# Kernel optimization log

Hardware: AMD Instinct MI355X
Metric: run time of the kernel (lower is better)

## Reference

```python
import jax, jax.numpy as jnp
import numpy as np

N, F, H, R, B, L, C, E, NB = 8192, 512, 256, 16, 32, 256, 7, 262144, 30
D = F + H


def setup_inputs() -> dict:
    ks = jax.random.split(jax.random.key(0), 16)
    g = lambda k, shape, fan: jax.random.normal(k, shape, jnp.float32) / np.sqrt(fan)
    return {
        "x": jax.random.normal(ks[0], (N, F), jnp.float32),
        "edge_index": jax.random.randint(ks[1], (2, E), 0, N),
        "edge_norm": jax.random.uniform(ks[2], (E,), jnp.float32),
        "edge_type": jax.random.randint(ks[3], (E,), 0, R),
        "seq_lengths": jnp.full((B,), L, dtype=jnp.int32),
        "umask": jnp.ones((B, L), jnp.float32),
        "nodal_attn": 1,
        "avec": 0,
        "basis": g(ks[4], (NB, F, H), F),
        "comp": g(ks[5], (R, NB), NB),
        "root1": g(ks[6], (F, H), F),
        "bias1": jnp.zeros((H,), jnp.float32),
        "w_rel": g(ks[7], (H, H), H),
        "b_rel": jnp.zeros((H,), jnp.float32),
        "w_root": g(ks[8], (H, H), H),
        "w_att": g(ks[9], (D, D), D),
        "b_att": jnp.zeros((D,), jnp.float32),
        "w_lin": g(ks[10], (D, H), D),
        "b_lin": jnp.zeros((H,), jnp.float32),
        "w_fc": g(ks[11], (H, C), H),
        "b_fc": jnp.zeros((C,), jnp.float32),
    }


def reference(x, edge_index, edge_norm, edge_type, seq_lengths, umask,
              nodal_attn, avec, basis, comp, root1, bias1, w_rel, b_rel,
              w_root, w_att, b_att, w_lin, b_lin, w_fc, b_fc):
    n = x.shape[0]
    r = comp.shape[0]
    src, dst = edge_index[0], edge_index[1]
    # ---- RGCNConv (num_bases basis decomposition, mean aggregation per relation, root + bias)
    W = jnp.einsum('rb,bfh->rfh', comp, basis)             # [R,F,H]
    xw = jnp.einsum('nf,rfh->nrh', x, W)                   # [N,R,H]
    msg = xw[src, edge_type]                               # [E,H] gather per edge
    seg = dst * r + edge_type                              # per (node, relation) segment
    cnt = jax.ops.segment_sum(jnp.ones((msg.shape[0],), msg.dtype), seg, num_segments=n * r)
    msg = msg / jnp.maximum(cnt[seg], 1.0)[:, None]
    out1 = jax.ops.segment_sum(msg, dst, num_segments=n) + x @ root1 + bias1
    # ---- GraphConv (add aggregation): W_rel * sum_j h_j + b_rel + W_root * h_i
    agg2 = jax.ops.segment_sum(out1[src], dst, num_segments=n)
    out2 = agg2 @ w_rel + b_rel + out1 @ w_root
    emotions = jnp.concatenate([x, out2], axis=-1)          # [N, F+H]
    if int(nodal_attn):
        seq = np.asarray(seq_lengths)                       # static conversation lengths
        starts = np.concatenate([[0], np.cumsum(seq)[:-1]])
        lmax = int(seq.max())
        rows = [jnp.pad(jax.lax.dynamic_slice_in_dim(emotions, int(s), int(l)),
                        ((0, lmax - int(l)), (0, 0)))
                for s, l in zip(starts, seq)]
        M = jnp.stack(rows, 0).transpose(1, 0, 2)           # [L, B, D]
        mask = umask                                        # [B, L]
        # MatchingAttention 'general2', vectorized over all timesteps t
        X = M @ w_att + b_att                               # transform(x_t) for every t: [L,B,D]
        Mm = M * mask.T[:, :, None]                         # mask memory over seq dim
        scores = jnp.einsum('tbd,sbd->tbs', X, Mm) * mask[None]
        a = jax.nn.softmax(jnp.tanh(scores), axis=-1) * mask[None]
        a = a / jnp.sum(a, axis=-1, keepdims=True)
        att = jnp.einsum('tbs,sbd->tbd', a, M)              # [L,B,D]
        hidden = jax.nn.relu(att @ w_lin + b_lin)
    else:
        hidden = jax.nn.relu(emotions @ w_lin + b_lin)
    # dropout is identity in eval mode
    logits = hidden @ w_fc + b_fc
    if int(avec):
        return logits
    return jax.nn.log_softmax(logits, axis=1)  # faithful: torch uses dim=1
```

## Files before the change

kernel.cpp:

```cpp
#include <hip/hip_runtime.h>
#include <hip/hip_bf16.h>

#define NN 8192
#define FF 512
#define HH 256
#define RR 16
#define BB 32
#define LL 256
#define CC 7
#define EE 262144
#define NBASE 30
#define DD 768

constexpr int FLAG_BIAS = 1, FLAG_RELU = 4, FLAG_TANH = 8,
              FLAG_SPLITOUT = 16, FLAG_TAILOUT = 32;

typedef __attribute__((ext_vector_type(8))) short bf16x8;
typedef __attribute__((ext_vector_type(4))) float f32x4;

__global__ __launch_bounds__(256) void detect_dtype(const unsigned short* __restrict__ xs,
                                                    int* __restrict__ flag) {
  __shared__ int red[256];
  int cnt = 0;
  for (int i = threadIdx.x * 2; i < 8192; i += 512) {
    unsigned short u = xs[i];
    int e = (u >> 7) & 0xFF;
    if (e >= 0xC0) cnt++;
  }
  red[threadIdx.x] = cnt;
  __syncthreads();
  for (int s = 128; s > 0; s >>= 1) {
    if (threadIdx.x < s) red[threadIdx.x] += red[threadIdx.x + s];
    __syncthreads();
  }
  if (threadIdx.x == 0) flag[0] = (red[0] > 16) ? 1 : 0;
}

struct ConvSeg {
  const void* src;
  float* dst;
  __hip_bfloat16* hi;
  __hip_bfloat16* lo;
  int n;
  int zero;
};
struct ConvTable {
  ConvSeg seg[12];
  int count;
  long total;
};

__global__ __launch_bounds__(256) void conv_all(ConvTable t, const int* __restrict__ flag) {
  const int fp32 = flag[0];
  for (long i = (long)blockIdx.x * 256 + threadIdx.x; i < t.total;
       i += (long)gridDim.x * 256) {
    long off = i;
    int s = 0;
    while (off >= t.seg[s].n) { off -= t.seg[s].n; s++; }
    const ConvSeg& sg = t.seg[s];
    float v = 0.f;
    if (!sg.zero)
      v = fp32 ? ((const float*)sg.src)[off]
               : __bfloat162float(((const __hip_bfloat16*)sg.src)[off]);
    if (sg.dst) sg.dst[off] = v;
    if (sg.hi) {
      __hip_bfloat16 h = __float2bfloat16(v);
      sg.hi[off] = h;
      sg.lo[off] = __float2bfloat16(v - __bfloat162float(h));
    }
  }
}

struct TSeg {
  const void* src;
  __hip_bfloat16* hi;
  __hip_bfloat16* lo;
  int R, C, ld, off;
};
struct TTable {
  TSeg seg[6];
  int count;
  long total;
};

__global__ __launch_bounds__(256) void split_t_all(TTable t, const int* __restrict__ flag) {
  const int fp32 = flag[0];
  for (long i = (long)blockIdx.x * 256 + threadIdx.x; i < t.total;
       i += (long)gridDim.x * 256) {
    long off = i;
    int s = 0;
    while (off >= (long)t.seg[s].R * t.seg[s].C) { off -= (long)t.seg[s].R * t.seg[s].C; s++; }
    const TSeg& sg = t.seg[s];
    int r = (int)(off % sg.R), c = (int)(off / sg.R);
    float v = fp32 ? ((const float*)sg.src)[(long)r * sg.C + c]
                   : __bfloat162float(((const __hip_bfloat16*)sg.src)[(long)r * sg.C + c]);
    __hip_bfloat16 h = __float2bfloat16(v);
    long d = (long)c * sg.ld + sg.off + r;
    sg.hi[d] = h;
    sg.lo[d] = __float2bfloat16(v - __bfloat162float(h));
  }
}

__global__ __launch_bounds__(256) void copy_xsplit(
    const __hip_bfloat16* __restrict__ xh, const __hip_bfloat16* __restrict__ xl,
    __hip_bfloat16* __restrict__ eh, __hip_bfloat16* __restrict__ el) {
  int idx = blockIdx.x * 256 + threadIdx.x;
  int n = idx >> 9, f = idx & 511;
  long d = (long)n * DD + f;
  eh[d] = xh[idx];
  el[d] = xl[idx];
}

__global__ __launch_bounds__(256) void transpose_b16(
    const __hip_bfloat16* __restrict__ src, __hip_bfloat16* __restrict__ dst) {
  __shared__ __hip_bfloat16 t[32][33];
  const long b = blockIdx.z;
  const int d0 = blockIdx.x * 32, s0 = blockIdx.y * 32;
  const int c = threadIdx.x & 31, rw = threadIdx.x >> 5;
  const __hip_bfloat16* sp = src + b * (LL * DD);
  __hip_bfloat16* dp = dst + b * (LL * DD);
#pragma unroll
  for (int i = 0; i < 4; ++i)
    t[rw + i * 8][c] = sp[(long)(s0 + rw + i * 8) * DD + d0 + c];
  __syncthreads();
#pragma unroll
  for (int i = 0; i < 4; ++i)
    dp[(long)(d0 + rw + i * 8) * LL + s0 + c] = t[c][rw + i * 8];
}

__global__ __launch_bounds__(256) void wt_gemm(
    const float* __restrict__ basis, const float* __restrict__ comp,
    float* __restrict__ wt_nat) {
  __shared__ float cs[RR * NBASE];
  int tid = threadIdx.x;
  for (int i = tid; i < RR * NBASE; i += 256) cs[i] = comp[i];
  __syncthreads();
  long col = (long)blockIdx.x * 256 + tid;
  float acc[RR] = {};
  for (int b = 0; b < NBASE; ++b) {
    float v = basis[(long)b * 131072 + col];
#pragma unroll
    for (int r = 0; r < RR; ++r) acc[r] += cs[r * NBASE + b] * v;
  }
#pragma unroll
  for (int r = 0; r < RR; ++r) wt_nat[(long)r * 131072 + col] = acc[r];
}

__global__ __launch_bounds__(256) void wt_transpose(
    const float* __restrict__ wt_nat,
    __hip_bfloat16* __restrict__ hi, __hip_bfloat16* __restrict__ lo) {
  __shared__ float t[32][33];
  const int r = blockIdx.z;
  const int f0 = blockIdx.y * 32, h0 = blockIdx.x * 32;
  const int c = threadIdx.x & 31, rw = threadIdx.x >> 5;
  const float* src = wt_nat + ((long)r * 512 + f0) * 256 + h0;
#pragma unroll
  for (int i = 0; i < 4; ++i)
    t[rw + i * 8][c] = src[(long)(rw + i * 8) * 256 + c];
  __syncthreads();
#pragma unroll
  for (int i = 0; i < 4; ++i) {
    int hh = rw + i * 8;
    float v = t[c][hh];
    long orow = (long)(r * 256 + h0 + hh) * 512 + f0 + c;
    __hip_bfloat16 hv = __float2bfloat16(v);
    hi[orow] = hv;
    lo[orow] = __float2bfloat16(v - __bfloat162float(hv));
  }
}

__device__ __forceinline__ void gload_lds16(const void* g, void* l) {
  __builtin_amdgcn_global_load_lds(
      (const __attribute__((address_space(1))) unsigned int*)g,
      (__attribute__((address_space(3))) unsigned int*)l, 16, 0, 0);
}

__global__ __launch_bounds__(256, 3) void mfma_dual(
    const __hip_bfloat16* __restrict__ A, const __hip_bfloat16* __restrict__ Alo,
    const __hip_bfloat16* __restrict__ Bt, const __hip_bfloat16* __restrict__ Btlo,
    const float* __restrict__ bias, float* __restrict__ C, float* __restrict__ Ct,
    __hip_bfloat16* __restrict__ Chi, __hip_bfloat16* __restrict__ Clo,
    int K, int ldc, long sA, long sB, long sC, int flags) {
  __shared__ __hip_bfloat16 Ah[128 * 32];
  __shared__ __hip_bfloat16 Bh[128 * 32];
  __shared__ __hip_bfloat16 Al[128 * 32];
  __shared__ __hip_bfloat16 Bl[128 * 32];
  const int tid = threadIdx.x;
  const int w = tid >> 6, lane = tid & 63;
  const long z = blockIdx.z;
  const long row0 = (long)blockIdx.y * 128, col0 = (long)blockIdx.x * 128;
  const int wm = w & 1, wn = w >> 1;
  const int srow0 = (w * 128 + lane) >> 2;
  const int srow1 = (w * 128 + 64 + lane) >> 2;
  const int kch = (lane & 3) * 8;
  const int fr = lane & 15, q = lane >> 4;
  const bool hasAlo = (Alo != nullptr);
  const __hip_bfloat16* Az = A + z * sA;
  const __hip_bfloat16* Alz = hasAlo ? (Alo + z * sA) : nullptr;
  const __hip_bfloat16* Bz = Bt + z * sB;
  const __hip_bfloat16* Blz = Btlo + z * sB;
  const long aoff0 = (row0 + srow0) * K + kch, aoff1 = (row0 + srow1) * K + kch;
  const long boff0 = (col0 + srow0) * K + kch, boff1 = (col0 + srow1) * K + kch;
  f32x4 acc[4][4] = {};
  for (int k0 = 0; k0 < K; k0 += 32) {
    gload_lds16(Az + aoff0 + k0, Ah + w * 1024);
    gload_lds16(Az + aoff1 + k0, Ah + w * 1024 + 512);
    gload_lds16(Bz + boff0 + k0, Bh + w * 1024);
    gload_lds16(Bz + boff1 + k0, Bh + w * 1024 + 512);
    gload_lds16(Blz + boff0 + k0, Bl + w * 1024);
    gload_lds16(Blz + boff1 + k0, Bl + w * 1024 + 512);
    if (hasAlo) {
      gload_lds16(Alz + aoff0 + k0, Al + w * 1024);
      gload_lds16(Alz + aoff1 + k0, Al + w * 1024 + 512);
    }
    __syncthreads();
    bf16x8 ah[4], bh[4], bl[4];
#pragma unroll
    for (int i = 0; i < 4; ++i) {
      ah[i] = *(const bf16x8*)&Ah[(wm * 64 + i * 16 + fr) * 32 + q * 8];
      bh[i] = *(const bf16x8*)&Bh[(wn * 64 + i * 16 + fr) * 32 + q * 8];
      bl[i] = *(const bf16x8*)&Bl[(wn * 64 + i * 16 + fr) * 32 + q * 8];
    }
#pragma unroll
    for (int i = 0; i < 4; ++i)
#pragma unroll
      for (int j = 0; j < 4; ++j) {
        acc[i][j] = __builtin_amdgcn_mfma_f32_16x16x32_bf16(ah[i], bh[j], acc[i][j], 0, 0, 0);
        acc[i][j] = __builtin_amdgcn_mfma_f32_16x16x32_bf16(ah[i], bl[j], acc[i][j], 0, 0, 0);
      }
    if (hasAlo) {
      bf16x8 al[4];
#pragma unroll
      for (int i = 0; i < 4; ++i)
        al[i] = *(const bf16x8*)&Al[(wm * 64 + i * 16 + fr) * 32 + q * 8];
#pragma unroll
      for (int i = 0; i < 4; ++i)
#pragma unroll
        for (int j = 0; j < 4; ++j)
          acc[i][j] = __builtin_amdgcn_mfma_f32_16x16x32_bf16(al[i], bh[j], acc[i][j], 0, 0, 0);
    }
    __syncthreads();
  }
  const int cr = (lane >> 4) * 4, cc = lane & 15;
  float* Cz = C ? (C + z * sC) : nullptr;
  __hip_bfloat16* Chz = Chi ? (Chi + z * sC) : nullptr;
  __hip_bfloat16* Clz = Clo ? (Clo + z * sC) : nullptr;
#pragma unroll
  for (int i = 0; i < 4; ++i) {
    long rbase = row0 + wm * 64 + i * 16 + cr;
#pragma unroll
    for (int j = 0; j < 4; ++j) {
      long col = col0 + wn * 64 + j * 16 + cc;
      float bv = (flags & FLAG_BIAS) ? bias[col] : 0.f;
#pragma unroll
      for (int r = 0; r < 4; ++r) {
        float v = acc[i][j][r] + bv;
        if (flags & FLAG_RELU) v = fmaxf(v, 0.f);
        if (flags & FLAG_TANH) v = tanhf(v);
        if (flags & FLAG_SPLITOUT) {
          long off = (rbase + r) * ldc + col;
          __hip_bfloat16 hv = __float2bfloat16(v);
          Chz[off] = hv;
          Clz[off] = __float2bfloat16(v - __bfloat162float(hv));
        } else if ((flags & FLAG_TAILOUT) && col >= 4096) {
          Ct[(rbase + r) * 256 + (col - 4096)] = v;
        } else {
          Cz[(rbase + r) * ldc + col] = v;
        }
      }
    }
  }
}

__global__ __launch_bounds__(256) void count_edges(
    const int* __restrict__ ei, const int* __restrict__ et, float* __restrict__ cnt) {
  int e = blockIdx.x * 256 + threadIdx.x;
  if (e < EE) atomicAdd(&cnt[ei[EE + e] * RR + et[e]], 1.0f);
}

__global__ __launch_bounds__(256) void scan_rowptr(
    const float* __restrict__ cntf, int* __restrict__ rowptr, int* __restrict__ fill) {
  __shared__ int part[256];
  int tid = threadIdx.x;
  int base = tid * 32;
  int local[32];
  int s = 0;
  for (int i = 0; i < 32; ++i) {
    local[i] = s;
    const float* c = &cntf[(base + i) * RR];
    int d = 0;
#pragma unroll
    for (int r = 0; r < RR; ++r) d += (int)c[r];
    s += d;
  }
  part[tid] = s;
  __syncthreads();
  for (int off = 1; off < 256; off <<= 1) {
    int v = (tid >= off) ? part[tid - off] : 0;
    __syncthreads();
    part[tid] += v;
    __syncthreads();
  }
  int prev = (tid == 0) ? 0 : part[tid - 1];
  for (int i = 0; i < 32; ++i) rowptr[base + i] = prev + local[i];
  if (tid == 255) rowptr[8192] = part[255];
  for (int i = tid; i < 8192; i += 256) fill[i] = 0;
}

__global__ __launch_bounds__(256) void edge_fill(
    const int* __restrict__ ei, const int* __restrict__ et,
    const int* __restrict__ rowptr, int* __restrict__ fill, int* __restrict__ eidx) {
  int e = blockIdx.x * 256 + threadIdx.x;
  if (e < EE) {
    int dst = ei[EE + e];
    int pos = rowptr[dst] + atomicAdd(&fill[dst], 1);
    eidx[pos] = ei[e] | (et[e] << 16);
  }
}

__global__ __launch_bounds__(256) void rgcn_gather(
    const int* __restrict__ rowptr, const int* __restrict__ eidx,
    const float* __restrict__ cntf, const float* __restrict__ xw,
    float* __restrict__ out1, __hip_bfloat16* __restrict__ a2o1_hi,
    __hip_bfloat16* __restrict__ a2o1_lo) {
  const int dst = blockIdx.x;
  const int h = threadIdx.x;
  __shared__ float inv[RR];
  __shared__ int se[256];
  if (h < RR) inv[h] = 1.0f / fmaxf(cntf[dst * RR + h], 1.0f);
  const int beg = rowptr[dst], end = rowptr[dst + 1];
  float acc = 0.f;
  for (int c0 = beg; c0 < end; c0 += 256) {
    int n = min(256, end - c0);
    __syncthreads();
    if (h < n) se[h] = eidx[c0 + h];
    __syncthreads();
    for (int i = 0; i < n; ++i) {
      int pk = se[i];
      int src = pk & 0xFFFF, r = pk >> 16;
      acc += xw[((long)src << 12) + (r << 8) + h] * inv[r];
    }
  }
  float tot = out1[((long)dst << 8) + h] + acc;
  out1[((long)dst << 8) + h] = tot;
  __hip_bfloat16 hv = __float2bfloat16(tot);
  long d = (long)dst * 512 + 256 + h;
  a2o1_hi[d] = hv;
  a2o1_lo[d] = __float2bfloat16(tot - __bfloat162float(hv));
}

__global__ __launch_bounds__(256) void graphconv_gather(
    const int* __restrict__ rowptr, const int* __restrict__ eidx,
    const float* __restrict__ out1, __hip_bfloat16* __restrict__ a2o1_hi,
    __hip_bfloat16* __restrict__ a2o1_lo) {
  const int dst = blockIdx.x;
  const int h = threadIdx.x;
  __shared__ int se[256];
  const int beg = rowptr[dst], end = rowptr[dst + 1];
  float acc = 0.f;
  for (int c0 = beg; c0 < end; c0 += 256) {
    int n = min(256, end - c0);
    __syncthreads();
    if (h < n) se[h] = eidx[c0 + h];
    __syncthreads();
    for (int i = 0; i < n; ++i)
      acc += out1[((long)(se[i] & 0xFFFF) << 8) + h];
  }
  __hip_bfloat16 hv = __float2bfloat16(acc);
  long d = (long)dst * 512 + h;
  a2o1_hi[d] = hv;
  a2o1_lo[d] = __float2bfloat16(acc - __bfloat162float(hv));
}

__global__ __launch_bounds__(256) void softmax256(const float* __restrict__ S,
                                                  __hip_bfloat16* __restrict__ Ab) {
  __shared__ float red[256];
  long row = blockIdx.x;
  const float* p = S + row * 256;
  int t = threadIdx.x;
  float v = p[t];
  red[t] = v;
  __syncthreads();
  for (int s = 128; s > 0; s >>= 1) {
    if (t < s) red[t] = fmaxf(red[t], red[t + s]);
    __syncthreads();
  }
  float m = red[0];
  __syncthreads();
  float e = __expf(v - m);
  red[t] = e;
  __syncthreads();
  for (int s = 128; s > 0; s >>= 1) {
    if (t < s) red[t] += red[t + s];
    __syncthreads();
  }
  Ab[row * 256 + t] = __float2bfloat16(e / red[0]);
}

__global__ __launch_bounds__(256) void logits_lsm(
    const float* __restrict__ hidden, const float* __restrict__ w_fc,
    const float* __restrict__ b_fc, void* __restrict__ out_v,
    const int* __restrict__ flag) {
  __shared__ float wf[256 * 7];
  __shared__ float lg[224];
  __shared__ float corr[7];
  int t = blockIdx.x;
  int tid = threadIdx.x;
  for (int i = tid; i < 256 * 7; i += 256) wf[i] = w_fc[i];
  __syncthreads();
  if (tid < 224) {
    int b = tid / 7, c = tid % 7;
    const float* hr = hidden + ((long)((b << 8) + t) << 8);
    float s = b_fc[c];
    for (int k = 0; k < 256; ++k) s += hr[k] * wf[k * 7 + c];
    lg[tid] = s;
  }
  __syncthreads();
  if (tid < 7) {
    float m = -1e30f;
    for (int b = 0; b < BB; ++b) m = fmaxf(m, lg[b * 7 + tid]);
    float sum = 0.f;
    for (int b = 0; b < BB; ++b) sum += __expf(lg[b * 7 + tid] - m);
    corr[tid] = m + logf(sum);
  }
  __syncthreads();
  if (tid < 224) {
    float v = lg[tid] - corr[tid % 7];
    if (flag[0]) ((float*)out_v)[t * 224 + tid] = v;
    else ((__hip_bfloat16*)out_v)[t * 224 + tid] = __float2bfloat16(v);
  }
}

extern "C" void kernel_launch(void* const* d_in, const int* in_sizes, int n_in,
                              void* d_out, int out_size, void* d_ws, size_t ws_size,
                              hipStream_t stream) {
  const int* ei = (const int*)d_in[1];
  const int* et = (const int*)d_in[3];

  float* ws = (float*)d_ws;
  int* flag = (int*)d_ws;
  float* p = ws + 16;
  auto alloc = [&](long nf) { float* r = p; p += nf; return r; };
  float* w_fc_f = alloc(1792);
  float* b_rel_f = alloc(256);
  float* biasx = alloc(4352);
  float* b_att_f = alloc(768);
  float* b_lin_f = alloc(256);
  float* b_fc_f = alloc(16);
  __hip_bfloat16* wlin_hi = (__hip_bfloat16*)alloc(98304);
  __hip_bfloat16* wlin_lo = (__hip_bfloat16*)alloc(98304);
  __hip_bfloat16* x_hi = (__hip_bfloat16*)alloc(2097152);
  __hip_bfloat16* x_lo = (__hip_bfloat16*)alloc(2097152);
  __hip_bfloat16* watt_hi = (__hip_bfloat16*)alloc(294912);
  __hip_bfloat16* watt_lo = (__hip_bfloat16*)alloc(294912);
  __hip_bfloat16* wrr_hi = (__hip_bfloat16*)alloc(65536);
  __hip_bfloat16* wrr_lo = (__hip_bfloat16*)alloc(65536);
  __hip_bfloat16* wtc_hi = (__hip_bfloat16*)alloc(1114112);
  __hip_bfloat16* wtc_lo = (__hip_bfloat16*)alloc(1114112);
  float* basis_f = alloc(3932160);
  float* comp_f = alloc(512);
  float* xw = alloc(33554432);
  float* cnt = alloc(131072);
  float* out1 = alloc(2097152);
  __hip_bfloat16* a2o1_hi = (__hip_bfloat16*)alloc(2097152);
  __hip_bfloat16* a2o1_lo = (__hip_bfloat16*)alloc(2097152);
  float* hidden = alloc(2097152);
  int* rowptr = (int*)alloc(8208);
  int* fillc = (int*)alloc(8192);
  int* eidx = (int*)alloc(262144);
  float* wt_nat = xw;
  float* em = xw;
  __hip_bfloat16* em_hi = (__hip_bfloat16*)(em + 6291456);
  __hip_bfloat16* em_lo = (__hip_bfloat16*)(em + 9437184);
  __hip_bfloat16* X_hi = (__hip_bfloat16*)(em + 12582912);
  __hip_bfloat16* X_lo = (__hip_bfloat16*)(em + 15728640);
  float* scores = em + 18874368;
  __hip_bfloat16* a_b16 = (__hip_bfloat16*)(em + 20971520);
  __hip_bfloat16* att_hi = (__hip_bfloat16*)(em + 22020096);
  __hip_bfloat16* att_lo = (__hip_bfloat16*)(em + 25165824);
  __hip_bfloat16* emT_hi = (__hip_bfloat16*)em;
  __hip_bfloat16* emT_lo = (__hip_bfloat16*)(em + 3145728);

  detect_dtype<<<1, 256, 0, stream>>>((const unsigned short*)d_in[0], flag);
  ConvTable T{};
  long tot = 0;
  int ns = 0;
  auto seg = [&](const void* s, float* d, __hip_bfloat16* hi, __hip_bfloat16* lo,
                 int n, int z) {
    T.seg[ns].src = s; T.seg[ns].dst = d; T.seg[ns].hi = hi; T.seg[ns].lo = lo;
    T.seg[ns].n = n; T.seg[ns].zero = z; ns++; tot += n;
  };
  seg(d_in[0], nullptr, x_hi, x_lo, NN * FF, 0);
  seg(d_in[8], basis_f, nullptr, nullptr, NBASE * FF * HH, 0);
  seg(d_in[9], comp_f, nullptr, nullptr, RR * NBASE, 0);
  seg(d_in[13], b_rel_f, nullptr, nullptr, HH, 0);
  seg(d_in[16], b_att_f, nullptr, nullptr, DD, 0);
  seg(d_in[18], b_lin_f, nullptr, nullptr, HH, 0);
  seg(d_in[19], w_fc_f, nullptr, nullptr, HH * CC, 0);
  seg(d_in[20], b_fc_f, nullptr, nullptr, CC, 0);
  seg(nullptr, biasx, nullptr, nullptr, 4096, 1);
  seg(d_in[11], biasx + 4096, nullptr, nullptr, HH, 0);
  T.count = ns;
  T.total = tot;
  conv_all<<<4096, 256, 0, stream>>>(T, flag);
  TTable TT{};
  long ttot = 0;
  int ts = 0;
  auto tseg = [&](const void* s, __hip_bfloat16* hi, __hip_bfloat16* lo,
                  int R, int C, int ld, int off) {
    TT.seg[ts].src = s; TT.seg[ts].hi = hi; TT.seg[ts].lo = lo;
    TT.seg[ts].R = R; TT.seg[ts].C = C; TT.seg[ts].ld = ld; TT.seg[ts].off = off;
    ts++; ttot += (long)R * C;
  };
  tseg(d_in[15], watt_hi, watt_lo, DD, DD, DD, 0);
  tseg(d_in[17], wlin_hi, wlin_lo, DD, HH, DD, 0);
  tseg(d_in[10], wtc_hi + 4096 * 512, wtc_lo + 4096 * 512, FF, HH, FF, 0);
  tseg(d_in[12], wrr_hi, wrr_lo, HH, HH, 512, 0);
  tseg(d_in[14], wrr_hi, wrr_lo, HH, HH, 512, 256);
  TT.count = ts;
  TT.total = ttot;
  split_t_all<<<2048, 256, 0, stream>>>(TT, flag);

  wt_gemm<<<131072 / 256, 256, 0, stream>>>(basis_f, comp_f, wt_nat);
  wt_transpose<<<dim3(8, 16, 16), 256, 0, stream>>>(wt_nat, wtc_hi, wtc_lo);
  mfma_dual<<<dim3(34, 64, 1), 256, 0, stream>>>(
      x_hi, x_lo, wtc_hi, wtc_lo, biasx, xw, out1, nullptr, nullptr, FF, 4096,
      0, 0, 0, FLAG_BIAS | FLAG_TAILOUT);
  hipMemsetAsync(cnt, 0, 131072 * sizeof(float), stream);
  count_edges<<<EE / 256, 256, 0, stream>>>(ei, et, cnt);
  scan_rowptr<<<1, 256, 0, stream>>>(cnt, rowptr, fillc);
  edge_fill<<<EE / 256, 256, 0, stream>>>(ei, et, rowptr, fillc, eidx);
  rgcn_gather<<<NN, 256, 0, stream>>>(rowptr, eidx, cnt, xw, out1, a2o1_hi, a2o1_lo);
  graphconv_gather<<<NN, 256, 0, stream>>>(rowptr, eidx, out1, a2o1_hi, a2o1_lo);
  copy_xsplit<<<(NN * FF) / 256, 256, 0, stream>>>(x_hi, x_lo, em_hi, em_lo);
  mfma_dual<<<dim3(2, 64, 1), 256, 0, stream>>>(
      a2o1_hi, a2o1_lo, wrr_hi, wrr_lo, b_rel_f, nullptr, nullptr,
      em_hi + 512, em_lo + 512, 512, DD, 0, 0, 0, FLAG_BIAS | FLAG_SPLITOUT);
  transpose_b16<<<dim3(24, 8, 32), 256, 0, stream>>>(em_hi, emT_hi);
  transpose_b16<<<dim3(24, 8, 32), 256, 0, stream>>>(em_lo, emT_lo);
  mfma_dual<<<dim3(6, 64, 1), 256, 0, stream>>>(
      em_hi, em_lo, watt_hi, watt_lo, b_att_f, nullptr, nullptr, X_hi, X_lo, DD, DD,
      0, 0, 0, FLAG_BIAS | FLAG_SPLITOUT);
  mfma_dual<<<dim3(2, 2, BB), 256, 0, stream>>>(
      X_hi, X_lo, em_hi, em_lo, nullptr, scores, nullptr, nullptr, nullptr, DD, LL,
      (long)LL * DD, (long)LL * DD, (long)LL * LL, FLAG_TANH);
  softmax256<<<BB * LL, 256, 0, stream>>>(scores, a_b16);
  mfma_dual<<<dim3(6, 2, BB), 256, 0, stream>>>(
      a_b16, nullptr, emT_hi, emT_lo, nullptr, nullptr, nullptr, att_hi, att_lo, LL, DD,
      (long)LL * LL, (long)LL * DD, (long)LL * DD, FLAG_SPLITOUT);
  mfma_dual<<<dim3(2, 64, 1), 256, 0, stream>>>(
      att_hi, att_lo, wlin_hi, wlin_lo, b_lin_f, hidden, nullptr, nullptr, nullptr,
      DD, HH, 0, 0, 0, FLAG_BIAS | FLAG_RELU);
  logits_lsm<<<LL, 256, 0, stream>>>(hidden, w_fc_f, b_fc_f, d_out, flag);
}
```

Baseline: 652.9 us.

## Reassociate attention output projection: multiply memory by w_lin before attention

Uses associativity (a @ M) @ w_lin = a @ (M @ w_lin): the memory is projected to 256 columns first, then transposed, and the batched attention GEMM yields hidden directly with bias and ReLU fused. This cuts the attention-weighted GEMM from 768 to 256 output columns and removes the separate att buffer and the final linear GEMM. The two transposes become one smaller launch over both hi and lo halves. Risk is a different rounding order, since the projected memory is stored as a bf16 hi/lo split.

After: 634.3 us. 2.8% less time.

```diff
diff --git a/kernel.cpp b/kernel.cpp
--- a/kernel.cpp
+++ b/kernel.cpp
@@ -111,21 +111,25 @@
   el[d] = xl[idx];
 }
 
-__global__ __launch_bounds__(256) void transpose_b16(
-    const __hip_bfloat16* __restrict__ src, __hip_bfloat16* __restrict__ dst) {
+__global__ __launch_bounds__(256) void transpose_emw(
+    const __hip_bfloat16* __restrict__ hi_src, const __hip_bfloat16* __restrict__ lo_src,
+    __hip_bfloat16* __restrict__ hi_dst, __hip_bfloat16* __restrict__ lo_dst) {
   __shared__ __hip_bfloat16 t[32][33];
-  const long b = blockIdx.z;
+  const int zz = blockIdx.z;
+  const __hip_bfloat16* src = (zz < 32) ? hi_src : lo_src;
+  __hip_bfloat16* dst = (zz < 32) ? hi_dst : lo_dst;
+  const long b = zz & 31;
   const int d0 = blockIdx.x * 32, s0 = blockIdx.y * 32;
   const int c = threadIdx.x & 31, rw = threadIdx.x >> 5;
-  const __hip_bfloat16* sp = src + b * (LL * DD);
-  __hip_bfloat16* dp = dst + b * (LL * DD);
+  const __hip_bfloat16* sp = src + b * (LL * 256);
+  __hip_bfloat16* dp = dst + b * (LL * 256);
 #pragma unroll
   for (int i = 0; i < 4; ++i)
-    t[rw + i * 8][c] = sp[(long)(s0 + rw + i * 8) * DD + d0 + c];
+    t[rw + i * 8][c] = sp[(long)(s0 + rw + i * 8) * 256 + d0 + c];
   __syncthreads();
 #pragma unroll
   for (int i = 0; i < 4; ++i)
-    dp[(long)(d0 + rw + i * 8) * LL + s0 + c] = t[c][rw + i * 8];
+    dp[(long)(d0 + rw + i * 8) * 256 + s0 + c] = t[c][rw + i * 8];
 }
 
 __global__ __launch_bounds__(256) void wt_gemm(
@@ -470,16 +474,16 @@
   int* eidx = (int*)alloc(262144);
   float* wt_nat = xw;
   float* em = xw;
+  __hip_bfloat16* emw_hi = (__hip_bfloat16*)em;
+  __hip_bfloat16* emw_lo = (__hip_bfloat16*)(em + 1048576);
+  __hip_bfloat16* emwT_hi = (__hip_bfloat16*)(em + 2097152);
+  __hip_bfloat16* emwT_lo = (__hip_bfloat16*)(em + 3145728);
   __hip_bfloat16* em_hi = (__hip_bfloat16*)(em + 6291456);
   __hip_bfloat16* em_lo = (__hip_bfloat16*)(em + 9437184);
   __hip_bfloat16* X_hi = (__hip_bfloat16*)(em + 12582912);
   __hip_bfloat16* X_lo = (__hip_bfloat16*)(em + 15728640);
   float* scores = em + 18874368;
   __hip_bfloat16* a_b16 = (__hip_bfloat16*)(em + 20971520);
-  __hip_bfloat16* att_hi = (__hip_bfloat16*)(em + 22020096);
-  __hip_bfloat16* att_lo = (__hip_bfloat16*)(em + 25165824);
-  __hip_bfloat16* emT_hi = (__hip_bfloat16*)em;
-  __hip_bfloat16* emT_lo = (__hip_bfloat16*)(em + 3145728);
 
   detect_dtype<<<1, 256, 0, stream>>>((const unsigned short*)d_in[0], flag);
   ConvTable T{};
@@ -536,8 +540,10 @@
   mfma_dual<<<dim3(2, 64, 1), 256, 0, stream>>>(
       a2o1_hi, a2o1_lo, wrr_hi, wrr_lo, b_rel_f, nullptr, nullptr,
       em_hi + 512, em_lo + 512, 512, DD, 0, 0, 0, FLAG_BIAS | FLAG_SPLITOUT);
-  transpose_b16<<<dim3(24, 8, 32), 256, 0, stream>>>(em_hi, emT_hi);
-  transpose_b16<<<dim3(24, 8, 32), 256, 0, stream>>>(em_lo, emT_lo);
+  mfma_dual<<<dim3(2, 64, 1), 256, 0, stream>>>(
+      em_hi, em_lo, wlin_hi, wlin_lo, nullptr, nullptr, nullptr, emw_hi, emw_lo,
+      DD, HH, 0, 0, 0, FLAG_SPLITOUT);
+  transpose_emw<<<dim3(8, 8, 64), 256, 0, stream>>>(emw_hi, emw_lo, emwT_hi, emwT_lo);
   mfma_dual<<<dim3(6, 64, 1), 256, 0, stream>>>(
       em_hi, em_lo, watt_hi, watt_lo, b_att_f, nullptr, nullptr, X_hi, X_lo, DD, DD,
       0, 0, 0, FLAG_BIAS | FLAG_SPLITOUT);
@@ -545,11 +551,8 @@
       X_hi, X_lo, em_hi, em_lo, nullptr, scores, nullptr, nullptr, nullptr, DD, LL,
       (long)LL * DD, (long)LL * DD, (long)LL * LL, FLAG_TANH);
   softmax256<<<BB * LL, 256, 0, stream>>>(scores, a_b16);
-  mfma_dual<<<dim3(6, 2, BB), 256, 0, stream>>>(
-      a_b16, nullptr, emT_hi, emT_lo, nullptr, nullptr, nullptr, att_hi, att_lo, LL, DD,
-      (long)LL * LL, (long)LL * DD, (long)LL * DD, FLAG_SPLITOUT);
-  mfma_dual<<<dim3(2, 64, 1), 256, 0, stream>>>(
-      att_hi, att_lo, wlin_hi, wlin_lo, b_lin_f, hidden, nullptr, nullptr, nullptr,
-      DD, HH, 0, 0, 0, FLAG_BIAS | FLAG_RELU);
+  mfma_dual<<<dim3(2, 2, BB), 256, 0, stream>>>(
+      a_b16, nullptr, emwT_hi, emwT_lo, b_lin_f, hidden, nullptr, nullptr, nullptr,
+      LL, HH, (long)LL * LL, (long)LL * HH, (long)LL * HH, FLAG_BIAS | FLAG_RELU);
   logits_lsm<<<LL, 256, 0, stream>>>(hidden, w_fc_f, b_fc_f, d_out, flag);
 }
```
